# Performance work log

Measured on AMD Instinct MI355X. Metric: run time of the kernel, lower is better.

## Reference

```python
import jax, jax.numpy as jnp
import numpy as np


def setup_inputs() -> dict:
    key = jax.random.key(0)
    ks = jax.random.split(key, 8)
    G, N = 64, 512          # num_graphs, nodes per subgraph (equal-size PyG Batch)
    total = G * N
    # location_info columns: [rb_x, rb_y, lt_x, lt_y, w, h, cx, cy, img_w, img_h]
    # keep all entries positive and away from 0 so log()/division are well-defined
    location_info = jax.random.uniform(ks[0], (total, 10), dtype=jnp.float32) + 0.5
    dims = [4, 64, 128, 256]
    def kaiming(k, out_d, in_d):
        return jax.random.normal(k, (out_d, in_d), dtype=jnp.float32) * jnp.sqrt(2.0 / in_d)
    return {
        "location_info": location_info,
        "W1": kaiming(ks[1], dims[1], dims[0]), "b1": jnp.zeros((dims[1],), jnp.float32),
        "W2": kaiming(ks[2], dims[2], dims[1]), "b2": jnp.zeros((dims[2],), jnp.float32),
        "W3": kaiming(ks[3], dims[3], dims[2]), "b3": jnp.zeros((dims[3],), jnp.float32),
        "num_graphs": G,
        "k": 16,
    }


def _knn_edges(location_info, num_graphs, k):
    """Per-subgraph Euclidean KNN (bt_cosine=False, no self loop, directed).
    Returns (src, tgt) flat node indices, 'source_to_target' flow."""
    total = location_info.shape[0]
    N = total // num_graphs
    pos = location_info[:, 6:8].reshape(num_graphs, N, 2)       # [G, N, 2]
    # pairwise squared distances [G, N, N]
    d2 = jnp.sum((pos[:, :, None, :] - pos[:, None, :, :]) ** 2, axis=-1)
    # exclude self (bt_self_loop=False)
    eye = jnp.eye(N, dtype=bool)
    d2 = jnp.where(eye[None, :, :], jnp.inf, d2)
    # k nearest neighbors of each node (row = query/target node)
    _, nbr = jax.lax.top_k(-d2, k)                               # [G, N, k]
    offs = (jnp.arange(num_graphs, dtype=jnp.int32) * N)[:, None, None]
    src = (nbr.astype(jnp.int32) + offs).reshape(-1)             # neighbors = sources
    tgt = jnp.broadcast_to(jnp.arange(N, dtype=jnp.int32)[None, :, None] + offs,
                           (num_graphs, N, k)).reshape(-1)       # centers = targets
    return src, tgt


def _edge_attr_imgnorm4(location_info, src, tgt):
    s = location_info[src]  # [E, 10]
    t = location_info[tgt]
    feat1 = (s[:, 6] - t[:, 6]) / s[:, 8]
    feat2 = (s[:, 7] - t[:, 7]) / s[:, 9]
    feat3 = jnp.log(s[:, 4] / t[:, 4])
    feat4 = jnp.log(s[:, 5] / t[:, 5])
    return jnp.stack([feat1, feat2, feat3, feat4], axis=1)       # [E, 4]


def _mlp(e, W1, b1, W2, b2, W3, b3):
    h = jax.nn.relu(e @ W1.T + b1)
    h = jax.nn.relu(h @ W2.T + b2)
    return jax.nn.relu(h @ W3.T + b3)                            # final_activation=True


def reference(location_info, W1, b1, W2, b2, W3, b3, num_graphs, k):
    src, tgt = _knn_edges(location_info, num_graphs, k)
    raw_edge_attr = _edge_attr_imgnorm4(location_info, src, tgt)
    edge_attr = _mlp(raw_edge_attr, W1, b1, W2, b2, W3, b3)
    edge_index = jnp.stack([src, tgt], axis=0)                   # [2, E]
    return edge_attr, edge_index
```

## Files before the change

kernel.cpp:

```cpp
#include <hip/hip_runtime.h>
#include <hip/hip_bf16.h>
#include <math.h>

#define G_NUM   64
#define N_NODES 512
#define K_NN    16
#define TOTAL   (G_NUM * N_NODES)
#define E_TOTAL (TOTAL * K_NN)
#define D0 4
#define D1 64
#define D2 128
#define D3 256

typedef _Float16 half8  __attribute__((ext_vector_type(8)));
typedef _Float16 half4t __attribute__((ext_vector_type(4)));
typedef _Float16 half2t __attribute__((ext_vector_type(2)));
typedef float    f32x4  __attribute__((ext_vector_type(4)));

__global__ __launch_bounds__(256) void knn_kernel(const float* __restrict__ loc,
                                                  const float* __restrict__ W2,
                                                  const float* __restrict__ W3,
                                                  _Float16* __restrict__ wsh,
                                                  float* __restrict__ out_ei) {
    __shared__ float posx[N_NODES];
    __shared__ float posy[N_NODES];
    __shared__ unsigned long long keys[32][8][17];

    const int g  = blockIdx.x;
    const int nb = blockIdx.y;
    const int t  = threadIdx.x;

    {
        const int gid = (g * 16 + nb) * 256 + t;
        if (gid < D2 * D1) wsh[gid] = (_Float16)W2[gid];
        else {
            const int j = gid - D2 * D1;
            if (j < D3 * D2) wsh[D2 * D1 + j] = (_Float16)W3[j];
        }
    }

    for (int i = t; i < N_NODES; i += 256) {
        const float* row = loc + (size_t)(g * N_NODES + i) * 10;
        posx[i] = row[6];
        posy[i] = row[7];
    }
    __syncthreads();

    const int ng = t >> 3;
    const int ch = t & 7;
    const int n  = nb * 32 + ng;

    const float px = posx[n];
    const float py = posy[n];

    float dist[K_NN];
    int   idx[K_NN];
#pragma unroll
    for (int j = 0; j < K_NN; ++j) { dist[j] = INFINITY; idx[j] = 0; }

    const int c0 = ch * 64;
    for (int cc = 0; cc < 64; ++cc) {
        const int c = c0 + cc;
        if (c == n) continue;
        const float dx = posx[c] - px;
        const float dy = posy[c] - py;
        const float d  = dx * dx + dy * dy;
        if (d < dist[K_NN - 1]) {
            dist[K_NN - 1] = d;
            idx[K_NN - 1]  = c;
#pragma unroll
            for (int j = K_NN - 1; j > 0; --j) {
                if (dist[j] < dist[j - 1]) {
                    float td = dist[j]; dist[j] = dist[j - 1]; dist[j - 1] = td;
                    int   ti = idx[j];  idx[j]  = idx[j - 1];  idx[j - 1]  = ti;
                }
            }
        }
    }

#pragma unroll
    for (int j = 0; j < K_NN; ++j)
        keys[ng][ch][j] = ((unsigned long long)__float_as_uint(dist[j]) << 32)
                          | (unsigned)idx[j];
    __syncthreads();

    int h = 0;
    float srcf[2];
    const int node  = g * N_NODES + n;
    const size_t eb = (size_t)node * K_NN;
#pragma unroll
    for (int j = 0; j < K_NN; ++j) {
        unsigned long long mykey = keys[ng][ch][h];
        unsigned long long win = mykey;
#pragma unroll
        for (int m = 1; m < 8; m <<= 1) {
            const unsigned long long o = __shfl_xor(win, m);
            win = (o < win) ? o : win;
        }
        if (mykey == win) ++h;
        if ((j >> 1) == ch)
            srcf[j & 1] = (float)(g * N_NODES + (int)(unsigned)(win & 0xffffffffu));
    }
    out_ei[eb + ch * 2]               = srcf[0];
    out_ei[eb + ch * 2 + 1]           = srcf[1];
    out_ei[E_TOTAL + eb + ch * 2]     = (float)node;
    out_ei[E_TOTAL + eb + ch * 2 + 1] = (float)node;
}

__device__ __forceinline__ int h1_ix(int r, int c) { return r * 64  + (c ^ ((r & 7) << 3)); }
__device__ __forceinline__ int h2_ix(int r, int c) { return r * 128 + (c ^ ((r & 7) << 3)); }

#define STG_W 264

__global__ __launch_bounds__(256) void mlp_kernel(const float* __restrict__ loc,
                                                  const float* __restrict__ ei_src,
                                                  const float* __restrict__ W1,
                                                  const float* __restrict__ b1,
                                                  const float* __restrict__ b2,
                                                  const float* __restrict__ b3,
                                                  const _Float16* __restrict__ wsh,
                                                  float* __restrict__ out) {
    __shared__ __align__(16) _Float16 h2s[64 * 128];
    __shared__ __align__(16) float    ovl[8 * STG_W];
    __shared__ __align__(16) float    feat[64][4];

    _Float16* h1s = (_Float16*)ovl;
    float (*stg)[STG_W] = (float(*)[STG_W])ovl;

    const int t = threadIdx.x;
    const int w = t >> 6;
    const int l = t & 63;
    const int lr = l & 15;
    const int lq = l >> 4;
    const size_t tile_base = (size_t)blockIdx.x * 64;

    const _Float16* w2h = wsh;
    const _Float16* w3h = wsh + D2 * D1;

    {
        const int e4 = t >> 2;
        const int f  = t & 3;
        const size_t e = tile_base + e4;
        const int src  = (int)ei_src[e];
        const int tgt  = (int)(e >> 4);
        const float* sr = loc + (size_t)src * 10;
        const float* tr = loc + (size_t)tgt * 10;
        const int ix = (f < 2) ? 6 + f : 2 + f;
        const float a = sr[ix];
        const float b = tr[ix];
        const float c = sr[8 + (f & 1)];
        float val;
        if (f < 2) val = (a - b) / c;
        else       val = logf(a / b);
        feat[e4][f] = val;
    }
    __syncthreads();

    {
        const f32x4 fv = *(const f32x4*)&feat[l][0];
#pragma unroll
        for (int u = 0; u < 8; ++u) {
            const int o0 = w * 16 + 2 * u;
            float a0 = b1[o0]     + fv[0] * W1[o0 * 4]     + fv[1] * W1[o0 * 4 + 1]
                                  + fv[2] * W1[o0 * 4 + 2] + fv[3] * W1[o0 * 4 + 3];
            float a1 = b1[o0 + 1] + fv[0] * W1[o0 * 4 + 4] + fv[1] * W1[o0 * 4 + 5]
                                  + fv[2] * W1[o0 * 4 + 6] + fv[3] * W1[o0 * 4 + 7];
            half2t p;
            p[0] = (_Float16)fmaxf(a0, 0.0f);
            p[1] = (_Float16)fmaxf(a1, 0.0f);
            *(half2t*)&h1s[h1_ix(l, o0)] = p;
        }
    }
    __syncthreads();

    {
        f32x4 bc2[2];
#pragma unroll
        for (int nn = 0; nn < 2; ++nn)
            bc2[nn] = *(const f32x4*)&b2[w * 32 + nn * 16 + lq * 4];

#pragma unroll
        for (int m = 0; m < 4; ++m) {
            f32x4 a2[2];
#pragma unroll
            for (int nn = 0; nn < 2; ++nn) a2[nn] = bc2[nn];
#pragma unroll
            for (int kt = 0; kt < 2; ++kt) {
                const half8 hf = *(const half8*)&h1s[h1_ix(m * 16 + lr, kt * 32 + lq * 8)];
#pragma unroll
                for (int nn = 0; nn < 2; ++nn) {
                    const half8 wf = *(const half8*)(w2h + (w * 32 + nn * 16 + lr) * D1 + kt * 32 + lq * 8);
                    a2[nn] = __builtin_amdgcn_mfma_f32_16x16x32_f16(wf, hf, a2[nn], 0, 0, 0);
                }
            }
#pragma unroll
            for (int nn = 0; nn < 2; ++nn) {
                half4t p;
#pragma unroll
                for (int r = 0; r < 4; ++r)
                    p[r] = (_Float16)fmaxf(a2[nn][r], 0.0f);
                *(half4t*)&h2s[h2_ix(m * 16 + lr, w * 32 + nn * 16 + lq * 4)] = p;
            }
        }
    }
    __syncthreads();

    {
        f32x4 bc3[4];
#pragma unroll
        for (int nn = 0; nn < 4; ++nn)
            bc3[nn] = *(const f32x4*)&b3[w * 64 + nn * 16 + lq * 4];

#pragma unroll
        for (int m = 0; m < 4; ++m) {
            f32x4 acc[4];
#pragma unroll
            for (int nn = 0; nn < 4; ++nn) acc[nn] = bc3[nn];
#pragma unroll
            for (int kt = 0; kt < 4; ++kt) {
                const half8 hf = *(const half8*)&h2s[h2_ix(m * 16 + lr, kt * 32 + lq * 8)];
#pragma unroll
                for (int nn = 0; nn < 4; ++nn) {
                    const half8 wf = *(const half8*)(w3h + (w * 64 + nn * 16 + lr) * D2 + kt * 32 + lq * 8);
                    acc[nn] = __builtin_amdgcn_mfma_f32_16x16x32_f16(wf, hf, acc[nn], 0, 0, 0);
                }
            }
#pragma unroll
            for (int hq = 0; hq < 2; ++hq) {
                __syncthreads();
                if ((lr >> 3) == hq) {
                    const int j = lr & 7;
#pragma unroll
                    for (int nn = 0; nn < 4; ++nn) {
                        f32x4 v;
#pragma unroll
                        for (int r = 0; r < 4; ++r)
                            v[r] = fmaxf(acc[nn][r], 0.0f);
                        *(f32x4*)&stg[j][w * 64 + nn * 16 + lq * 4] = v;
                    }
                }
                __syncthreads();
#pragma unroll
                for (int jj = 0; jj < 2; ++jj) {
                    const int j = w * 2 + jj;
                    const size_t e = tile_base + m * 16 + hq * 8 + j;
                    const f32x4 v = *(const f32x4*)&stg[j][l * 4];
                    *(f32x4*)(out + e * D3 + l * 4) = v;
                }
            }
        }
    }
}

extern "C" void kernel_launch(void* const* d_in, const int* in_sizes, int n_in,
                              void* d_out, int out_size, void* d_ws, size_t ws_size,
                              hipStream_t stream) {
    const float* loc = (const float*)d_in[0];
    const float* W1  = (const float*)d_in[1];
    const float* b1  = (const float*)d_in[2];
    const float* W2  = (const float*)d_in[3];
    const float* b2  = (const float*)d_in[4];
    const float* W3  = (const float*)d_in[5];
    const float* b3  = (const float*)d_in[6];
    float* out = (float*)d_out;

    float* out_ei = out + (size_t)E_TOTAL * D3;
    _Float16* wsh = (_Float16*)d_ws;

    hipLaunchKernelGGL(knn_kernel, dim3(G_NUM, 16), dim3(256), 0, stream,
                       loc, W2, W3, wsh, out_ei);
    hipLaunchKernelGGL(mlp_kernel, dim3(E_TOTAL / 64), dim3(256), 0, stream,
                       loc, out_ei, W1, b1, b2, b3, wsh, out);
}
```

Before: 193.3 us.

## Compute all layer-3 tiles first, then double-buffer output staging

Restructures the third MLP layer to accumulate all four 16-row M tiles into registers (loop order kt outer, m inner) before any output. The output write-out then alternates between two staging buffers, reusing the freed h2s region as the second buffer. This roughly halves the number of __syncthreads in the store phase and lets staging writes overlap global stores. In exchange, register pressure rises to 64 f32 accumulators per thread, which may lower occupancy or cause spills.

```diff
diff --git a/kernel.cpp b/kernel.cpp
--- a/kernel.cpp
+++ b/kernel.cpp
@@ -125,7 +125,8 @@
     __shared__ __align__(16) float    feat[64][4];
 
     _Float16* h1s = (_Float16*)ovl;
-    float (*stg)[STG_W] = (float(*)[STG_W])ovl;
+    float (*stgA)[STG_W] = (float(*)[STG_W])ovl;
+    float (*stgB)[STG_W] = (float(*)[STG_W])h2s;
 
     const int t = threadIdx.x;
     const int w = t >> 6;
@@ -205,6 +206,7 @@
     }
     __syncthreads();
 
+    f32x4 acc[4][4];
     {
         f32x4 bc3[4];
 #pragma unroll
@@ -212,43 +214,65 @@
             bc3[nn] = *(const f32x4*)&b3[w * 64 + nn * 16 + lq * 4];
 
 #pragma unroll
-        for (int m = 0; m < 4; ++m) {
-            f32x4 acc[4];
-#pragma unroll
-            for (int nn = 0; nn < 4; ++nn) acc[nn] = bc3[nn];
-#pragma unroll
-            for (int kt = 0; kt < 4; ++kt) {
+        for (int m = 0; m < 4; ++m)
+#pragma unroll
+            for (int nn = 0; nn < 4; ++nn) acc[m][nn] = bc3[nn];
+
+#pragma unroll
+        for (int kt = 0; kt < 4; ++kt) {
+#pragma unroll
+            for (int m = 0; m < 4; ++m) {
                 const half8 hf = *(const half8*)&h2s[h2_ix(m * 16 + lr, kt * 32 + lq * 8)];
 #pragma unroll
                 for (int nn = 0; nn < 4; ++nn) {
                     const half8 wf = *(const half8*)(w3h + (w * 64 + nn * 16 + lr) * D2 + kt * 32 + lq * 8);
-                    acc[nn] = __builtin_amdgcn_mfma_f32_16x16x32_f16(wf, hf, acc[nn], 0, 0, 0);
-                }
-            }
-#pragma unroll
-            for (int hq = 0; hq < 2; ++hq) {
-                __syncthreads();
-                if ((lr >> 3) == hq) {
-                    const int j = lr & 7;
-#pragma unroll
-                    for (int nn = 0; nn < 4; ++nn) {
-                        f32x4 v;
-#pragma unroll
-                        for (int r = 0; r < 4; ++r)
-                            v[r] = fmaxf(acc[nn][r], 0.0f);
-                        *(f32x4*)&stg[j][w * 64 + nn * 16 + lq * 4] = v;
-                    }
-                }
-                __syncthreads();
-#pragma unroll
-                for (int jj = 0; jj < 2; ++jj) {
-                    const int j = w * 2 + jj;
-                    const size_t e = tile_base + m * 16 + hq * 8 + j;
-                    const f32x4 v = *(const f32x4*)&stg[j][l * 4];
-                    *(f32x4*)(out + e * D3 + l * 4) = v;
-                }
-            }
-        }
+                    acc[m][nn] = __builtin_amdgcn_mfma_f32_16x16x32_f16(wf, hf, acc[m][nn], 0, 0, 0);
+                }
+            }
+        }
+    }
+    __syncthreads();
+
+    if ((lr >> 3) == 0) {
+        const int j = lr & 7;
+#pragma unroll
+        for (int nn = 0; nn < 4; ++nn) {
+            f32x4 v;
+#pragma unroll
+            for (int r = 0; r < 4; ++r) v[r] = fmaxf(acc[0][nn][r], 0.0f);
+            *(f32x4*)&stgA[j][w * 64 + nn * 16 + lq * 4] = v;
+        }
+    }
+    __syncthreads();
+
+#pragma unroll
+    for (int q = 0; q < 8; ++q) {
+        if (q + 1 < 8) {
+            const int mq = (q + 1) >> 1;
+            const int hq = (q + 1) & 1;
+            if ((lr >> 3) == hq) {
+                const int j = lr & 7;
+                float (*stgN)[STG_W] = ((q + 1) & 1) ? stgB : stgA;
+#pragma unroll
+                for (int nn = 0; nn < 4; ++nn) {
+                    f32x4 v;
+#pragma unroll
+                    for (int r = 0; r < 4; ++r) v[r] = fmaxf(acc[mq][nn][r], 0.0f);
+                    *(f32x4*)&stgN[j][w * 64 + nn * 16 + lq * 4] = v;
+                }
+            }
+        }
+        {
+            float (*stgC)[STG_W] = (q & 1) ? stgB : stgA;
+#pragma unroll
+            for (int jj = 0; jj < 2; ++jj) {
+                const int j = w * 2 + jj;
+                const size_t e = tile_base + q * 8 + j;
+                const f32x4 v = *(const f32x4*)&stgC[j][l * 4];
+                *(f32x4*)(out + e * D3 + l * 4) = v;
+            }
+        }
+        __syncthreads();
     }
 }
 
```

Measured after the change: 196.3 us. About the same (+1.6%).

## Fuse KNN selection into MLP kernel using wave-wide iterative min selection

Applied to the files above, without the earlier changes.

Moves the per-node KNN search into the MLP kernel. Each wave computes distances for one target node across 64 lanes and picks the 16 nearest by repeated wave-wide min reductions, and the source indices go straight to shared memory instead of being written to and read back from global memory. Weight prepacking becomes a separate small kernel. The cost is that each block reloads its subgraph's 512 positions and runs 16 rounds of 64-bit shuffle reductions, which is redundant work repeated across the 128 blocks of each graph.

```diff
diff --git a/kernel.cpp b/kernel.cpp
--- a/kernel.cpp
+++ b/kernel.cpp
@@ -17,94 +17,13 @@
 typedef _Float16 half2t __attribute__((ext_vector_type(2)));
 typedef float    f32x4  __attribute__((ext_vector_type(4)));
 
-__global__ __launch_bounds__(256) void knn_kernel(const float* __restrict__ loc,
-                                                  const float* __restrict__ W2,
-                                                  const float* __restrict__ W3,
-                                                  _Float16* __restrict__ wsh,
-                                                  float* __restrict__ out_ei) {
-    __shared__ float posx[N_NODES];
-    __shared__ float posy[N_NODES];
-    __shared__ unsigned long long keys[32][8][17];
-
-    const int g  = blockIdx.x;
-    const int nb = blockIdx.y;
-    const int t  = threadIdx.x;
-
-    {
-        const int gid = (g * 16 + nb) * 256 + t;
-        if (gid < D2 * D1) wsh[gid] = (_Float16)W2[gid];
-        else {
-            const int j = gid - D2 * D1;
-            if (j < D3 * D2) wsh[D2 * D1 + j] = (_Float16)W3[j];
-        }
-    }
-
-    for (int i = t; i < N_NODES; i += 256) {
-        const float* row = loc + (size_t)(g * N_NODES + i) * 10;
-        posx[i] = row[6];
-        posy[i] = row[7];
-    }
-    __syncthreads();
-
-    const int ng = t >> 3;
-    const int ch = t & 7;
-    const int n  = nb * 32 + ng;
-
-    const float px = posx[n];
-    const float py = posy[n];
-
-    float dist[K_NN];
-    int   idx[K_NN];
-#pragma unroll
-    for (int j = 0; j < K_NN; ++j) { dist[j] = INFINITY; idx[j] = 0; }
-
-    const int c0 = ch * 64;
-    for (int cc = 0; cc < 64; ++cc) {
-        const int c = c0 + cc;
-        if (c == n) continue;
-        const float dx = posx[c] - px;
-        const float dy = posy[c] - py;
-        const float d  = dx * dx + dy * dy;
-        if (d < dist[K_NN - 1]) {
-            dist[K_NN - 1] = d;
-            idx[K_NN - 1]  = c;
-#pragma unroll
-            for (int j = K_NN - 1; j > 0; --j) {
-                if (dist[j] < dist[j - 1]) {
-                    float td = dist[j]; dist[j] = dist[j - 1]; dist[j - 1] = td;
-                    int   ti = idx[j];  idx[j]  = idx[j - 1];  idx[j - 1]  = ti;
-                }
-            }
-        }
-    }
-
-#pragma unroll
-    for (int j = 0; j < K_NN; ++j)
-        keys[ng][ch][j] = ((unsigned long long)__float_as_uint(dist[j]) << 32)
-                          | (unsigned)idx[j];
-    __syncthreads();
-
-    int h = 0;
-    float srcf[2];
-    const int node  = g * N_NODES + n;
-    const size_t eb = (size_t)node * K_NN;
-#pragma unroll
-    for (int j = 0; j < K_NN; ++j) {
-        unsigned long long mykey = keys[ng][ch][h];
-        unsigned long long win = mykey;
-#pragma unroll
-        for (int m = 1; m < 8; m <<= 1) {
-            const unsigned long long o = __shfl_xor(win, m);
-            win = (o < win) ? o : win;
-        }
-        if (mykey == win) ++h;
-        if ((j >> 1) == ch)
-            srcf[j & 1] = (float)(g * N_NODES + (int)(unsigned)(win & 0xffffffffu));
-    }
-    out_ei[eb + ch * 2]               = srcf[0];
-    out_ei[eb + ch * 2 + 1]           = srcf[1];
-    out_ei[E_TOTAL + eb + ch * 2]     = (float)node;
-    out_ei[E_TOTAL + eb + ch * 2 + 1] = (float)node;
+__global__ __launch_bounds__(256) void prepack_kernel(const float* __restrict__ W2,
+                                                      const float* __restrict__ W3,
+                                                      _Float16* __restrict__ wsh) {
+    const int i = blockIdx.x * 256 + threadIdx.x;
+    if (i < D2 * D1) wsh[i] = (_Float16)W2[i];
+    const int j = i - D2 * D1;
+    if (j >= 0 && j < D3 * D2) wsh[D2 * D1 + j] = (_Float16)W3[j];
 }
 
 __device__ __forceinline__ int h1_ix(int r, int c) { return r * 64  + (c ^ ((r & 7) << 3)); }
@@ -112,17 +31,21 @@
 
 #define STG_W 264
 
-__global__ __launch_bounds__(256) void mlp_kernel(const float* __restrict__ loc,
-                                                  const float* __restrict__ ei_src,
-                                                  const float* __restrict__ W1,
-                                                  const float* __restrict__ b1,
-                                                  const float* __restrict__ b2,
-                                                  const float* __restrict__ b3,
-                                                  const _Float16* __restrict__ wsh,
-                                                  float* __restrict__ out) {
+__global__ __launch_bounds__(256) void fused_kernel(const float* __restrict__ loc,
+                                                    const float* __restrict__ W1,
+                                                    const float* __restrict__ b1,
+                                                    const float* __restrict__ b2,
+                                                    const float* __restrict__ b3,
+                                                    const _Float16* __restrict__ wsh,
+                                                    float* __restrict__ out,
+                                                    float* __restrict__ out_ei) {
     __shared__ __align__(16) _Float16 h2s[64 * 128];
     __shared__ __align__(16) float    ovl[8 * STG_W];
     __shared__ __align__(16) float    feat[64][4];
+    __shared__ int edge_src[4][16];
+
+    float* posx = (float*)h2s;
+    float* posy = posx + N_NODES;
 
     _Float16* h1s = (_Float16*)ovl;
     float (*stg)[STG_W] = (float(*)[STG_W])ovl;
@@ -132,17 +55,71 @@
     const int l = t & 63;
     const int lr = l & 15;
     const int lq = l >> 4;
-    const size_t tile_base = (size_t)blockIdx.x * 64;
+    const int bid = blockIdx.x;
+    const int g = bid >> 7;
+    const int node0 = (bid & 127) * 4;
+    const size_t tile_base = (size_t)bid * 64;
 
     const _Float16* w2h = wsh;
     const _Float16* w3h = wsh + D2 * D1;
 
+    for (int i = t; i < N_NODES; i += 256) {
+        const float* row = loc + (size_t)(g * N_NODES + i) * 10;
+        posx[i] = row[6];
+        posy[i] = row[7];
+    }
+    __syncthreads();
+
+    {
+        const int n = node0 + w;
+        const float px = posx[n];
+        const float py = posy[n];
+
+        unsigned long long k8[8];
+#pragma unroll
+        for (int cc = 0; cc < 8; ++cc) {
+            const int c = l * 8 + cc;
+            const float dx = posx[c] - px;
+            const float dy = posy[c] - py;
+            const float d  = dx * dx + dy * dy;
+            const unsigned long long key =
+                ((unsigned long long)__float_as_uint(d) << 32) | (unsigned)c;
+            k8[cc] = (c == n) ? ~0ULL : key;
+        }
+
+        unsigned long long winkey = 0;
+#pragma unroll
+        for (int it = 0; it < K_NN; ++it) {
+            unsigned long long lmin = k8[0];
+#pragma unroll
+            for (int j = 1; j < 8; ++j) lmin = (k8[j] < lmin) ? k8[j] : lmin;
+            unsigned long long win = lmin;
+#pragma unroll
+            for (int m = 1; m < 64; m <<= 1) {
+                const unsigned long long o = __shfl_xor(win, m);
+                win = (o < win) ? o : win;
+            }
+#pragma unroll
+            for (int j = 0; j < 8; ++j)
+                if (k8[j] == win) k8[j] = ~0ULL;
+            if (l == it) winkey = win;
+        }
+
+        if (l < K_NN) {
+            const int src_g  = g * N_NODES + (int)(unsigned)(winkey & 0xffffffffu);
+            const int node_g = g * N_NODES + n;
+            edge_src[w][l] = src_g;
+            out_ei[(size_t)node_g * K_NN + l]           = (float)src_g;
+            out_ei[E_TOTAL + (size_t)node_g * K_NN + l] = (float)node_g;
+        }
+    }
+    __syncthreads();
+
     {
         const int e4 = t >> 2;
         const int f  = t & 3;
-        const size_t e = tile_base + e4;
-        const int src  = (int)ei_src[e];
-        const int tgt  = (int)(e >> 4);
+        const int src  = edge_src[e4 >> 4][e4 & 15];
+        const int tgt  = g * N_NODES + node0 + (e4 >> 4);
         const float* sr = loc + (size_t)src * 10;
         const float* tr = loc + (size_t)tgt * 10;
         const int ix = (f < 2) ? 6 + f : 2 + f;
@@ -267,8 +244,7 @@
     float* out_ei = out + (size_t)E_TOTAL * D3;
     _Float16* wsh = (_Float16*)d_ws;
 
-    hipLaunchKernelGGL(knn_kernel, dim3(G_NUM, 16), dim3(256), 0, stream,
-                       loc, W2, W3, wsh, out_ei);
-    hipLaunchKernelGGL(mlp_kernel, dim3(E_TOTAL / 64), dim3(256), 0, stream,
-                       loc, out_ei, W1, b1, b2, b3, wsh, out);
+    hipLaunchKernelGGL(prepack_kernel, dim3(160), dim3(256), 0, stream, W2, W3, wsh);
+    hipLaunchKernelGGL(fused_kernel, dim3(TOTAL / 4), dim3(256), 0, stream,
+                       loc, W1, b1, b2, b3, wsh, out, out_ei);
 }
```

Result: slower. 232.4 us (+20.3%).
